# Optimization experiments

Hardware: AMD Instinct MI355X
Metric: run time of the kernel (lower is better)

The kernel has to match this reference:

```python
import jax, jax.numpy as jnp
import numpy as np

N_NODES = 50000
N_EDGES = 800000


def spmm(edge_src, edge_dst, edge_weight, h):
    # out[i] = sum over edges (src->dst=i) of w * h[src]  == adj @ h
    msgs = h[edge_src] * edge_weight[:, None]  # [E, D]
    return jax.ops.segment_sum(msgs, edge_dst, num_segments=N_NODES)


def setup_inputs() -> dict:
    key = jax.random.key(0)
    ks = jax.random.split(key, 12)
    x = jax.random.normal(ks[0], (N_NODES, 512), dtype=jnp.float32)
    edge_src = jax.random.randint(ks[1], (N_EDGES,), 0, N_NODES, dtype=jnp.int32)
    edge_dst = jax.random.randint(ks[2], (N_EDGES,), 0, N_NODES, dtype=jnp.int32)
    edge_weight = jax.random.uniform(ks[3], (N_EDGES,), dtype=jnp.float32)
    def init_w(k, fin, fout):
        s = 1.0 / np.sqrt(fout)
        return jax.random.uniform(k, (fin, fout), minval=-s, maxval=s, dtype=jnp.float32)
    W1 = init_w(ks[4], 512, 512); b1 = jnp.zeros((512,), jnp.float32)
    W2 = init_w(ks[5], 512, 256); b2 = jnp.zeros((256,), jnp.float32)
    W3 = init_w(ks[6], 256, 128); b3 = jnp.zeros((128,), jnp.float32)
    W4 = init_w(ks[7], 128, 64);  b4 = jnp.zeros((64,), jnp.float32)
    return {"x": x, "edge_src": edge_src, "edge_dst": edge_dst,
            "edge_weight": edge_weight, "W1": W1, "b1": b1, "W2": W2,
            "b2": b2, "W3": W3, "b3": b3, "W4": W4, "b4": b4}


def reference(x, edge_src, edge_dst, edge_weight, W1, b1, W2, b2, W3, b3, W4, b4):
    # GraphConvolution: out = adj @ (x @ W) + b ; dropout is identity in eval mode
    def gc(h, W, b):
        return spmm(edge_src, edge_dst, edge_weight, h @ W) + b
    h = jax.nn.relu(gc(x, W1, b1))
    h = jax.nn.relu(gc(h, W2, b2))
    h = jax.nn.relu(gc(h, W3, b3))
    emb = gc(h, W4, b4)
    return emb
```

## Files before the change

kernel.cpp:

```cpp
#include <hip/hip_runtime.h>

#define NN 50000
#define NE 800000
#define SCAN_BLOCKS 196
#define CVT_BLOCKS 12800
#define HIST_BLOCKS 3125

typedef __attribute__((ext_vector_type(8))) short short8;
typedef __attribute__((ext_vector_type(4))) float float4v;

struct __align__(8) us4 { unsigned short x, y, z, w; };
struct __align__(16) us8 { unsigned short v[8]; };

__device__ __forceinline__ unsigned short f2bf(float f) {
    unsigned u = __float_as_uint(f);
    unsigned r = (u + 0x7FFF + ((u >> 16) & 1)) >> 16;
    return (unsigned short)r;
}

__device__ __forceinline__ float bf2f(unsigned short u) {
    return __uint_as_float((unsigned)u << 16);
}

__device__ __forceinline__ void gload_lds16(const unsigned short* g, unsigned short* l) {
    __builtin_amdgcn_global_load_lds(
        (const __attribute__((address_space(1))) unsigned int*)g,
        (__attribute__((address_space(3))) unsigned int*)l,
        16, 0, 0);
}

template <int BM, int BN, int WM, int WN, int OUTBF>
__global__ __launch_bounds__(256) void gemm_mfma(const unsigned short* __restrict__ A,
                                                 const unsigned short* __restrict__ Bt,
                                                 void* __restrict__ Cv,
                                                 int N, int K, int M) {
    constexpr int BK = 32;
    constexpr int MT = WM / 16;
    constexpr int NT = WN / 16;
    constexpr int WCOLS = BN / WN;

    __shared__ __align__(16) unsigned short As[2][BM * BK];
    __shared__ __align__(16) unsigned short Bs[2][BN * BK];

    const int tid = threadIdx.x;
    const int lane = tid & 63;
    const int wid = tid >> 6;
    const int col16 = lane & 15;
    const int q = lane >> 4;
    const int wr = (wid / WCOLS) * WM;
    const int wc = (wid % WCOLS) * WN;
    const int rowBase = blockIdx.x * BM;
    const int colBase = blockIdx.y * BN;

    const int srow = lane >> 2;
    const int scol = (lane & 3) * 8;

    float4v acc[MT][NT];
#pragma unroll
    for (int t = 0; t < MT; ++t)
#pragma unroll
        for (int u = 0; u < NT; ++u)
            acc[t][u] = (float4v)0.f;

    auto stage = [&](int buf, int k0) {
#pragma unroll
        for (int l = wid; l < BM / 16; l += 4) {
            int row = rowBase + 16 * l + srow;
            row = row < N ? row : N - 1;
            gload_lds16(A + (size_t)row * K + k0 + scol, &As[buf][l * 512]);
        }
#pragma unroll
        for (int l = wid; l < BN / 16; l += 4) {
            const int row = colBase + 16 * l + srow;
            gload_lds16(Bt + (size_t)row * K + k0 + scol, &Bs[buf][l * 512]);
        }
    };

    auto compute = [&](int buf) {
        short8 a[MT], b[NT];
#pragma unroll
        for (int t = 0; t < MT; ++t)
            a[t] = *(const short8*)&As[buf][(wr + t * 16 + col16) * BK + q * 8];
#pragma unroll
        for (int u = 0; u < NT; ++u)
            b[u] = *(const short8*)&Bs[buf][(wc + u * 16 + col16) * BK + q * 8];
#pragma unroll
        for (int t = 0; t < MT; ++t)
#pragma unroll
            for (int u = 0; u < NT; ++u)
                acc[t][u] = __builtin_amdgcn_mfma_f32_16x16x32_bf16(a[t], b[u], acc[t][u], 0, 0, 0);
    };

    stage(0, 0);
    __syncthreads();
    int cur = 0;
    for (int k0 = BK; k0 < K; k0 += BK) {
        stage(cur ^ 1, k0);
        compute(cur);
        __syncthreads();
        cur ^= 1;
    }
    compute(cur);

#pragma unroll
    for (int t = 0; t < MT; ++t) {
        const int row0 = rowBase + wr + t * 16 + q * 4;
#pragma unroll
        for (int u = 0; u < NT; ++u) {
            const int col = colBase + wc + u * 16 + col16;
#pragma unroll
            for (int r = 0; r < 4; ++r) {
                const int row = row0 + r;
                if (row < N) {
                    if (OUTBF)
                        ((unsigned short*)Cv)[(size_t)row * M + col] = f2bf(acc[t][u][r]);
                    else
                        ((float*)Cv)[(size_t)row * M + col] = acc[t][u][r];
                }
            }
        }
    }
}

__global__ void cvt_hist(const float* __restrict__ in, unsigned short* __restrict__ out,
                         const int* __restrict__ dst, int* __restrict__ counts) {
    const int b = blockIdx.x;
    if (b < CVT_BLOCKS) {
        const long long n4 = (long long)NN * 512 / 4;
        long long i = (long long)b * 256 + threadIdx.x;
        const long long stride = (long long)CVT_BLOCKS * 256;
        for (; i < n4; i += stride) {
            const float4 v = *(const float4*)&in[i * 4];
            us4 o = {f2bf(v.x), f2bf(v.y), f2bf(v.z), f2bf(v.w)};
            *(us4*)&out[i * 4] = o;
        }
    } else {
        int i = (b - CVT_BLOCKS) * 256 + threadIdx.x;
        const int stride = HIST_BLOCKS * 256;
        for (; i < NE; i += stride) atomicAdd(&counts[dst[i]], 1);
    }
}

__global__ void cvt_transpose_all(const float* __restrict__ W1, unsigned short* __restrict__ Wt1,
                                  const float* __restrict__ W2, unsigned short* __restrict__ Wt2,
                                  const float* __restrict__ W3, unsigned short* __restrict__ Wt3,
                                  const float* __restrict__ W4, unsigned short* __restrict__ Wt4) {
    int idx = blockIdx.x * blockDim.x + threadIdx.x;
    const float* W; unsigned short* Wt; int K, M;
    if (idx < 262144)      { W = W1; Wt = Wt1; K = 512; M = 512; }
    else if (idx < 393216) { idx -= 262144; W = W2; Wt = Wt2; K = 512; M = 256; }
    else if (idx < 425984) { idx -= 393216; W = W3; Wt = Wt3; K = 256; M = 128; }
    else if (idx < 434176) { idx -= 425984; W = W4; Wt = Wt4; K = 128; M = 64; }
    else return;
    const int k = idx / M;
    const int m = idx % M;
    Wt[(size_t)m * K + k] = f2bf(W[(size_t)k * M + m]);
}

__global__ void zero_counts(int* __restrict__ counts) {
    int i = blockIdx.x * blockDim.x + threadIdx.x;
    if (i < NN) counts[i] = 0;
}

__global__ __launch_bounds__(256) void scan_partial(const int* __restrict__ counts,
                                                    int* __restrict__ partials) {
    __shared__ int r[256];
    const int t = threadIdx.x;
    const int i = blockIdx.x * 256 + t;
    r[t] = (i < NN) ? counts[i] : 0;
    __syncthreads();
    for (int s = 128; s > 0; s >>= 1) {
        if (t < s) r[t] += r[t + s];
        __syncthreads();
    }
    if (t == 0) partials[blockIdx.x] = r[0];
}

__global__ __launch_bounds__(256) void scan_base(const int* __restrict__ partials,
                                                 int* __restrict__ bases,
                                                 int* __restrict__ offs) {
    __shared__ int s[256];
    const int t = threadIdx.x;
    const int v = (t < SCAN_BLOCKS) ? partials[t] : 0;
    s[t] = v;
    __syncthreads();
    for (int off = 1; off < 256; off <<= 1) {
        int x = (t >= off) ? s[t - off] : 0;
        __syncthreads();
        s[t] += x;
        __syncthreads();
    }
    if (t < SCAN_BLOCKS) bases[t] = s[t] - v;
    if (t == 255) offs[NN] = s[255];
}

__global__ __launch_bounds__(256) void scan_final(int* __restrict__ counts,
                                                  const int* __restrict__ bases,
                                                  int* __restrict__ offs) {
    __shared__ int s[256];
    const int t = threadIdx.x;
    const int i = blockIdx.x * 256 + t;
    const int v = (i < NN) ? counts[i] : 0;
    s[t] = v;
    __syncthreads();
    for (int off = 1; off < 256; off <<= 1) {
        int x = (t >= off) ? s[t - off] : 0;
        __syncthreads();
        s[t] += x;
        __syncthreads();
    }
    if (i < NN) {
        const int e = bases[blockIdx.x] + s[t] - v;
        offs[i] = e;
        counts[i] = e;
    }
}

__global__ void fill_csr(const int* __restrict__ src, const int* __restrict__ dst,
                         const float* __restrict__ w, int* __restrict__ cursor,
                         int2* __restrict__ csr) {
    int i = blockIdx.x * blockDim.x + threadIdx.x;
    const int stride = gridDim.x * blockDim.x;
    for (; i < NE; i += stride) {
        const int p = atomicAdd(&cursor[dst[i]], 1);
        csr[p] = make_int2(src[i], __float_as_int(w[i]));
    }
}

template <int D, int RELU, int OUTBF>
__global__ __launch_bounds__(256) void spmm_gather(const int* __restrict__ offs,
                                                   const int2* __restrict__ csr,
                                                   const unsigned short* __restrict__ hp,
                                                   const float* __restrict__ bias,
                                                   void* __restrict__ outv,
                                                   int dbase, int dstride) {
    constexpr int TPN = D / 8;
    constexpr int NPB = 256 / TPN;
    const int tid = threadIdx.x;
    const int node = blockIdx.x * NPB + tid / TPN;
    const int d = dbase + (tid % TPN) * 8;
    if (node >= NN) return;
    const int beg = offs[node];
    const int end = offs[node + 1];

    float acc[8] = {};
    int j = beg;
    for (; j + 8 <= end; j += 8) {
        int2 e[8];
#pragma unroll
        for (int t = 0; t < 8; ++t) e[t] = csr[j + t];
        us8 h[8];
#pragma unroll
        for (int t = 0; t < 8; ++t)
            h[t] = *(const us8*)&hp[(long long)e[t].x * dstride + d];
#pragma unroll
        for (int t = 0; t < 8; ++t) {
            const float w = __int_as_float(e[t].y);
#pragma unroll
            for (int k = 0; k < 8; ++k) acc[k] += w * bf2f(h[t].v[k]);
        }
    }
    for (; j + 2 <= end; j += 2) {
        const int2 e0 = csr[j];
        const int2 e1 = csr[j + 1];
        const us8 h0 = *(const us8*)&hp[(long long)e0.x * dstride + d];
        const us8 h1 = *(const us8*)&hp[(long long)e1.x * dstride + d];
        const float w0 = __int_as_float(e0.y);
        const float w1 = __int_as_float(e1.y);
#pragma unroll
        for (int k = 0; k < 8; ++k)
            acc[k] += w0 * bf2f(h0.v[k]) + w1 * bf2f(h1.v[k]);
    }
    if (j < end) {
        const int2 e0 = csr[j];
        const us8 h0 = *(const us8*)&hp[(long long)e0.x * dstride + d];
        const float w0 = __int_as_float(e0.y);
#pragma unroll
        for (int k = 0; k < 8; ++k) acc[k] += w0 * bf2f(h0.v[k]);
    }
#pragma unroll
    for (int k = 0; k < 8; ++k) {
        acc[k] += bias[d + k];
        if (RELU) acc[k] = fmaxf(acc[k], 0.f);
    }
    if (OUTBF) {
        us8 o;
#pragma unroll
        for (int k = 0; k < 8; ++k) o.v[k] = f2bf(acc[k]);
        *(us8*)((unsigned short*)outv + (long long)node * dstride + d) = o;
    } else {
        float* op = (float*)outv + (long long)node * dstride + d;
        *(float4*)op = make_float4(acc[0], acc[1], acc[2], acc[3]);
        *(float4*)(op + 4) = make_float4(acc[4], acc[5], acc[6], acc[7]);
    }
}

extern "C" void kernel_launch(void* const* d_in, const int* in_sizes, int n_in,
                              void* d_out, int out_size, void* d_ws, size_t ws_size,
                              hipStream_t stream) {
    const float* x    = (const float*)d_in[0];
    const int*   esrc = (const int*)d_in[1];
    const int*   edst = (const int*)d_in[2];
    const float* ew   = (const float*)d_in[3];
    const float* W1 = (const float*)d_in[4];  const float* b1 = (const float*)d_in[5];
    const float* W2 = (const float*)d_in[6];  const float* b2 = (const float*)d_in[7];
    const float* W3 = (const float*)d_in[8];  const float* b3 = (const float*)d_in[9];
    const float* W4 = (const float*)d_in[10]; const float* b4 = (const float*)d_in[11];
    float* out = (float*)d_out;

    char* ws = (char*)d_ws;
    int*   offs    = (int*)ws;                    ws += (NN + 1) * sizeof(int);
    int*   counts  = (int*)ws;                    ws += NN * sizeof(int);
    int*   partials= (int*)ws;                    ws += 256 * sizeof(int);
    int*   bases   = (int*)ws;                    ws += 256 * sizeof(int);
    ws = (char*)(((uintptr_t)ws + 15) & ~(uintptr_t)15);
    int2*  csr     = (int2*)ws;                   ws += (size_t)NE * sizeof(int2);
    unsigned short* Wt1 = (unsigned short*)ws;    ws += 512 * 512 * sizeof(unsigned short);
    unsigned short* Wt2 = (unsigned short*)ws;    ws += 256 * 512 * sizeof(unsigned short);
    unsigned short* Wt3 = (unsigned short*)ws;    ws += 128 * 256 * sizeof(unsigned short);
    unsigned short* Wt4 = (unsigned short*)ws;    ws += 64 * 128 * sizeof(unsigned short);
    ws = (char*)(((uintptr_t)ws + 255) & ~(uintptr_t)255);
    unsigned short* tmp = (unsigned short*)ws;    ws += (size_t)NN * 512 * sizeof(unsigned short);
    ws = (char*)(((uintptr_t)ws + 255) & ~(uintptr_t)255);
    unsigned short* hb = (unsigned short*)ws;

    zero_counts<<<(NN + 255) / 256, 256, 0, stream>>>(counts);
    cvt_hist<<<CVT_BLOCKS + HIST_BLOCKS, 256, 0, stream>>>(x, hb, edst, counts);
    scan_partial<<<SCAN_BLOCKS, 256, 0, stream>>>(counts, partials);
    scan_base<<<1, 256, 0, stream>>>(partials, bases, offs);
    scan_final<<<SCAN_BLOCKS, 256, 0, stream>>>(counts, bases, offs);
    fill_csr<<<3125, 256, 0, stream>>>(esrc, edst, ew, counts, csr);
    cvt_transpose_all<<<(434176 + 255) / 256, 256, 0, stream>>>(W1, Wt1, W2, Wt2, W3, Wt3, W4, Wt4);

    const int nby128 = (NN + 127) / 128;
    const int nby64  = (NN + 63) / 64;

    gemm_mfma<128, 128, 64, 64, 1><<<dim3(nby128, 4), 256, 0, stream>>>(hb, Wt1, tmp, NN, 512, 512);
    spmm_gather<256, 1, 1><<<NN / 8, 256, 0, stream>>>(offs, csr, tmp, b1, hb, 0, 512);
    spmm_gather<256, 1, 1><<<NN / 8, 256, 0, stream>>>(offs, csr, tmp, b1, hb, 256, 512);
    gemm_mfma<128, 128, 64, 64, 1><<<dim3(nby128, 2), 256, 0, stream>>>(hb, Wt2, tmp, NN, 512, 256);
    spmm_gather<256, 1, 1><<<NN / 8, 256, 0, stream>>>(offs, csr, tmp, b2, hb, 0, 256);
    gemm_mfma<64, 128, 32, 64, 1><<<dim3(nby64, 1), 256, 0, stream>>>(hb, Wt3, tmp, NN, 256, 128);
    spmm_gather<128, 1, 1><<<NN / 16, 256, 0, stream>>>(offs, csr, tmp, b3, hb, 0, 128);
    gemm_mfma<64, 64, 32, 32, 1><<<dim3(nby64, 1), 256, 0, stream>>>(hb, Wt4, tmp, NN, 128, 64);
    spmm_gather<64, 0, 0><<<(NN + 31) / 32, 256, 0, stream>>>(offs, csr, tmp, b4, out, 0, 64);
}
```

Baseline: 613.9 us.

## Pad atomic counters, interleave hist/convert blocks, merge first-layer spmm passes

Each node's degree counter now sits on its own 64-byte stride (CPAD=16), so the histogram and CSR fill atomics stop contending on shared cache lines. Histogram blocks are interleaved with conversion blocks (every fifth block) so atomic work spreads across the dispatch instead of trailing at the end. The two half-width spmm passes for layer 1 become a single full 512-wide gather, so edge lists and CSR entries are read once instead of twice. In exchange the counter array grows 16x and the scans read it with a strided, uncoalesced pattern.

```diff
diff --git a/kernel.cpp b/kernel.cpp
--- a/kernel.cpp
+++ b/kernel.cpp
@@ -3,8 +3,7 @@
 #define NN 50000
 #define NE 800000
 #define SCAN_BLOCKS 196
-#define CVT_BLOCKS 12800
-#define HIST_BLOCKS 3125
+#define CPAD 16
 
 typedef __attribute__((ext_vector_type(8))) short short8;
 typedef __attribute__((ext_vector_type(4))) float float4v;
@@ -122,22 +121,25 @@
     }
 }
 
+#define CH_BLOCKS 16000
 __global__ void cvt_hist(const float* __restrict__ in, unsigned short* __restrict__ out,
                          const int* __restrict__ dst, int* __restrict__ counts) {
     const int b = blockIdx.x;
-    if (b < CVT_BLOCKS) {
+    if ((b % 5) != 4) {
+        const int cb = (b / 5) * 4 + (b % 5);
         const long long n4 = (long long)NN * 512 / 4;
-        long long i = (long long)b * 256 + threadIdx.x;
-        const long long stride = (long long)CVT_BLOCKS * 256;
+        long long i = (long long)cb * 256 + threadIdx.x;
+        const long long stride = 12800LL * 256;
         for (; i < n4; i += stride) {
             const float4 v = *(const float4*)&in[i * 4];
             us4 o = {f2bf(v.x), f2bf(v.y), f2bf(v.z), f2bf(v.w)};
             *(us4*)&out[i * 4] = o;
         }
     } else {
-        int i = (b - CVT_BLOCKS) * 256 + threadIdx.x;
-        const int stride = HIST_BLOCKS * 256;
-        for (; i < NE; i += stride) atomicAdd(&counts[dst[i]], 1);
+        const int hb = b / 5;
+        int i = hb * 256 + threadIdx.x;
+        const int stride = 3200 * 256;
+        for (; i < NE; i += stride) atomicAdd(&counts[(size_t)dst[i] * CPAD], 1);
     }
 }
 
@@ -157,9 +159,9 @@
     Wt[(size_t)m * K + k] = f2bf(W[(size_t)k * M + m]);
 }
 
-__global__ void zero_counts(int* __restrict__ counts) {
+__global__ void zero_counts_pad(int4* __restrict__ counts4) {
     int i = blockIdx.x * blockDim.x + threadIdx.x;
-    if (i < NN) counts[i] = 0;
+    if (i < NN * CPAD / 4) counts4[i] = make_int4(0, 0, 0, 0);
 }
 
 __global__ __launch_bounds__(256) void scan_partial(const int* __restrict__ counts,
@@ -167,7 +169,7 @@
     __shared__ int r[256];
     const int t = threadIdx.x;
     const int i = blockIdx.x * 256 + t;
-    r[t] = (i < NN) ? counts[i] : 0;
+    r[t] = (i < NN) ? counts[(size_t)i * CPAD] : 0;
     __syncthreads();
     for (int s = 128; s > 0; s >>= 1) {
         if (t < s) r[t] += r[t + s];
@@ -200,7 +202,7 @@
     __shared__ int s[256];
     const int t = threadIdx.x;
     const int i = blockIdx.x * 256 + t;
-    const int v = (i < NN) ? counts[i] : 0;
+    const int v = (i < NN) ? counts[(size_t)i * CPAD] : 0;
     s[t] = v;
     __syncthreads();
     for (int off = 1; off < 256; off <<= 1) {
@@ -212,7 +214,7 @@
     if (i < NN) {
         const int e = bases[blockIdx.x] + s[t] - v;
         offs[i] = e;
-        counts[i] = e;
+        counts[(size_t)i * CPAD] = e;
     }
 }
 
@@ -222,7 +224,7 @@
     int i = blockIdx.x * blockDim.x + threadIdx.x;
     const int stride = gridDim.x * blockDim.x;
     for (; i < NE; i += stride) {
-        const int p = atomicAdd(&cursor[dst[i]], 1);
+        const int p = atomicAdd(&cursor[(size_t)dst[i] * CPAD], 1);
         csr[p] = make_int2(src[i], __float_as_int(w[i]));
     }
 }
@@ -310,10 +312,10 @@
 
     char* ws = (char*)d_ws;
     int*   offs    = (int*)ws;                    ws += (NN + 1) * sizeof(int);
-    int*   counts  = (int*)ws;                    ws += NN * sizeof(int);
     int*   partials= (int*)ws;                    ws += 256 * sizeof(int);
     int*   bases   = (int*)ws;                    ws += 256 * sizeof(int);
-    ws = (char*)(((uintptr_t)ws + 15) & ~(uintptr_t)15);
+    ws = (char*)(((uintptr_t)ws + 63) & ~(uintptr_t)63);
+    int*   counts  = (int*)ws;                    ws += (size_t)NN * CPAD * sizeof(int);
     int2*  csr     = (int2*)ws;                   ws += (size_t)NE * sizeof(int2);
     unsigned short* Wt1 = (unsigned short*)ws;    ws += 512 * 512 * sizeof(unsigned short);
     unsigned short* Wt2 = (unsigned short*)ws;    ws += 256 * 512 * sizeof(unsigned short);
@@ -324,8 +326,8 @@
     ws = (char*)(((uintptr_t)ws + 255) & ~(uintptr_t)255);
     unsigned short* hb = (unsigned short*)ws;
 
-    zero_counts<<<(NN + 255) / 256, 256, 0, stream>>>(counts);
-    cvt_hist<<<CVT_BLOCKS + HIST_BLOCKS, 256, 0, stream>>>(x, hb, edst, counts);
+    zero_counts_pad<<<(NN * CPAD / 4 + 255) / 256, 256, 0, stream>>>((int4*)counts);
+    cvt_hist<<<CH_BLOCKS, 256, 0, stream>>>(x, hb, edst, counts);
     scan_partial<<<SCAN_BLOCKS, 256, 0, stream>>>(counts, partials);
     scan_base<<<1, 256, 0, stream>>>(partials, bases, offs);
     scan_final<<<SCAN_BLOCKS, 256, 0, stream>>>(counts, bases, offs);
@@ -336,8 +338,7 @@
     const int nby64  = (NN + 63) / 64;
 
     gemm_mfma<128, 128, 64, 64, 1><<<dim3(nby128, 4), 256, 0, stream>>>(hb, Wt1, tmp, NN, 512, 512);
-    spmm_gather<256, 1, 1><<<NN / 8, 256, 0, stream>>>(offs, csr, tmp, b1, hb, 0, 512);
-    spmm_gather<256, 1, 1><<<NN / 8, 256, 0, stream>>>(offs, csr, tmp, b1, hb, 256, 512);
+    spmm_gather<512, 1, 1><<<NN / 4, 256, 0, stream>>>(offs, csr, tmp, b1, hb, 0, 512);
     gemm_mfma<128, 128, 64, 64, 1><<<dim3(nby128, 2), 256, 0, stream>>>(hb, Wt2, tmp, NN, 512, 256);
     spmm_gather<256, 1, 1><<<NN / 8, 256, 0, stream>>>(offs, csr, tmp, b2, hb, 0, 256);
     gemm_mfma<64, 128, 32, 64, 1><<<dim3(nby64, 1), 256, 0, stream>>>(hb, Wt3, tmp, NN, 256, 128);
```

Result: faster. 572.0 us (-6.8%).
